# Performance work log

Hardware: AMD Instinct MI355X
Metric: run time of the kernel (lower is better)

Reference implementation:

```python
import jax, jax.numpy as jnp
import numpy as np

B, N, H, D = 8, 2048, 8, 64  # batch, seq, heads, head_dim
DM = H * D                   # model dim = 512


def setup_inputs() -> dict:
    key = jax.random.key(0)
    ks = jax.random.split(key, 9)
    std = 0.02
    return {
        "x": jax.random.normal(ks[0], (B, N, DM), dtype=jnp.float32),
        "Wq": jax.random.normal(ks[1], (H, D, D), dtype=jnp.float32) * std,
        "bq": jnp.zeros((H, D), dtype=jnp.float32),
        "Wk": jax.random.normal(ks[2], (H, D, D), dtype=jnp.float32) * std,
        "bk": jnp.zeros((H, D), dtype=jnp.float32),
        "Wv": jax.random.normal(ks[3], (H, D, D), dtype=jnp.float32) * std,
        "bv": jnp.zeros((H, D), dtype=jnp.float32),
        "Wp": jax.random.normal(ks[4], (DM, DM), dtype=jnp.float32) * std,
        "bp": jnp.zeros((DM,), dtype=jnp.float32),
    }


def reference(x, Wq, bq, Wk, bk, Wv, bv, Wp, bp):
    b, n, dm = x.shape
    # rearrange 'b n (h d) -> b h n d'
    xh = x.reshape(b, n, H, D).transpose(0, 2, 1, 3)  # [b,h,n,d]
    # per-head linear projections (torch Linear: y = x W^T + b), batched over heads
    q = jnp.einsum('bhnd,hed->bhne', xh, Wq) + bq[None, :, None, :]
    k = jnp.einsum('bhnd,hed->bhne', xh, Wk) + bk[None, :, None, :]
    v = jnp.einsum('bhnd,hed->bhne', xh, Wv) + bv[None, :, None, :]
    scale = 1.0 / jnp.sqrt(jnp.asarray(D, dtype=x.dtype))
    scores = jnp.einsum('bhqe,bhke->bhqk', q, k) * scale  # [b,h,n,n]
    attn = jax.nn.softmax(scores, axis=-1)
    out = jnp.einsum('bhqk,bhke->bhqe', attn, v)          # [b,h,n,d]
    # 'b h n d -> b n (h d)' then output projection
    out = out.transpose(0, 2, 1, 3).reshape(b, n, H * D)
    return out @ Wp.T + bp
```

## Files before the change

### kernel.cpp

```cpp
#include <hip/hip_runtime.h>
#include <hip/hip_bf16.h>

#define B_ 8
#define N_ 2048
#define H_ 8
#define DM_ 512
#define NT_ 32

typedef __bf16 bf16x8 __attribute__((ext_vector_type(8)));
typedef float f32x4 __attribute__((ext_vector_type(4)));
typedef float f32x16 __attribute__((ext_vector_type(16)));
typedef unsigned short us8 __attribute__((ext_vector_type(8)));
typedef unsigned short us4 __attribute__((ext_vector_type(4)));
typedef unsigned int u32x4 __attribute__((ext_vector_type(4)));

#define QSCALE 0.1803368801111204f

__device__ __forceinline__ int swz(int row, int byte_in_row) {
  return row * 128 + (byte_in_row ^ ((row & 7) << 4));
}

__device__ __forceinline__ unsigned short f2bf(float x) {
  __bf16 h = (__bf16)x;
  return __builtin_bit_cast(unsigned short, h);
}

__device__ __forceinline__ float fexp2(float x) {
#if __has_builtin(__builtin_amdgcn_exp2f)
  return __builtin_amdgcn_exp2f(x);
#else
  return exp2f(x);
#endif
}

__device__ __forceinline__ unsigned cvtpk(float a, float b) {
  unsigned r;
  asm("v_cvt_pk_bf16_f32 %0, %1, %2" : "=v"(r) : "v"(a), "v"(b));
  return r;
}

__device__ __forceinline__ void plswap(unsigned& a, unsigned& b) {
#if __has_builtin(__builtin_amdgcn_permlane32_swap)
  auto r = __builtin_amdgcn_permlane32_swap(a, b, false, false);
  a = r[0];
  b = r[1];
#else
  asm("v_permlane32_swap_b32 %0, %1" : "+v"(a), "+v"(b));
#endif
}

__device__ __forceinline__ f32x4 mfma16(bf16x8 a, bf16x8 b, f32x4 c) {
  return __builtin_amdgcn_mfma_f32_16x16x32_bf16(a, b, c, 0, 0, 0);
}
__device__ __forceinline__ f32x16 mfma32(bf16x8 a, bf16x8 b, f32x16 c) {
  return __builtin_amdgcn_mfma_f32_32x32x16_bf16(a, b, c, 0, 0, 0);
}

__device__ __forceinline__ bf16x8 ldg8(const unsigned short* p) {
  return *reinterpret_cast<const bf16x8*>(p);
}

__device__ __forceinline__ void stage_f32_tile(const float* __restrict__ src,
                                               int src_stride, char* dst, int t) {
#pragma unroll
  for (int rep = 0; rep < 4; ++rep) {
    int cid = rep * 256 + t;
    int row = cid >> 4, c4 = cid & 15;
    float4 v = *reinterpret_cast<const float4*>(src + (size_t)row * src_stride + c4 * 4);
    us4 o;
    o[0] = f2bf(v.x); o[1] = f2bf(v.y); o[2] = f2bf(v.z); o[3] = f2bf(v.w);
    *reinterpret_cast<us4*>(dst + row * 128 + ((c4 * 8) ^ ((row & 7) << 4))) = o;
  }
}

__device__ __forceinline__ void stage_bf16_tile(const unsigned short* __restrict__ src,
                                                int src_stride, char* dst, int t) {
#pragma unroll
  for (int rep = 0; rep < 2; ++rep) {
    int cid = rep * 256 + t;
    int row = cid >> 3, c = cid & 7;
    us8 v = *reinterpret_cast<const us8*>(src + (size_t)row * src_stride + c * 8);
    *reinterpret_cast<us8*>(dst + row * 128 + ((c * 16) ^ ((row & 7) << 4))) = v;
  }
}

__global__ __launch_bounds__(256, 4) void qkv_kernel(
    const float* __restrict__ x,
    const float* __restrict__ Wq, const float* __restrict__ bq,
    const float* __restrict__ Wk, const float* __restrict__ bk,
    const float* __restrict__ Wv, const float* __restrict__ bv,
    unsigned short* __restrict__ Qf, unsigned short* __restrict__ Kf,
    unsigned short* __restrict__ Vf) {
  __shared__ __align__(16) char sX[8192];
  __shared__ __align__(16) char sWq[8192];
  __shared__ __align__(16) char sWk[8192];
  __shared__ __align__(16) char sWv[8192];

  const int t = threadIdx.x;
  const int bh = blockIdx.y, h = bh & 7, b = bh >> 3;
  const int n0 = blockIdx.x * 64;
  const int lane = t & 63, w = t >> 6, g = lane >> 4, li = lane & 15;

  stage_f32_tile(x + ((size_t)(b * N_ + n0)) * DM_ + h * 64, DM_, sX, t);
  stage_f32_tile(Wq + (size_t)h * 4096, 64, sWq, t);
  stage_f32_tile(Wk + (size_t)h * 4096, 64, sWk, t);
  stage_f32_tile(Wv + (size_t)h * 4096, 64, sWv, t);
  __syncthreads();

  bf16x8 xa0 = *reinterpret_cast<const bf16x8*>(sX + swz(16 * w + li, 16 * g));
  bf16x8 xa1 = *reinterpret_cast<const bf16x8*>(sX + swz(16 * w + li, 64 + 16 * g));

  const size_t seg = (size_t)N_ * 64;
  const int qkbase =
      ((n0 >> 5) + (w >> 1)) * 2048 + (li >> 3) * 256 + (w & 1) * 128 + (li & 7);
  const int vbase =
      (n0 >> 6) * 4096 + w * 512 + (g >> 1) * 256 + 4 * (g & 1) + li * 8;

  unsigned short* Qs = Qf + (size_t)bh * seg;
  unsigned short* Ks = Kf + (size_t)bh * seg;
  unsigned short* Vs = Vf + (size_t)bh * seg;

#pragma unroll
  for (int c = 0; c < 4; ++c) {
    f32x4 a = {0.f, 0.f, 0.f, 0.f};
    bf16x8 b0 = *reinterpret_cast<const bf16x8*>(sWq + swz(c * 16 + li, 16 * g));
    bf16x8 b1 = *reinterpret_cast<const bf16x8*>(sWq + swz(c * 16 + li, 64 + 16 * g));
    a = mfma16(xa0, b0, a);
    a = mfma16(xa1, b1, a);
    float bb = bq[h * 64 + c * 16 + li];
#pragma unroll
    for (int i = 0; i < 4; ++i)
      Qs[qkbase + c * 512 + (4 * g + i) * 8] = f2bf((a[i] + bb) * QSCALE);
  }
#pragma unroll
  for (int c = 0; c < 4; ++c) {
    f32x4 a = {0.f, 0.f, 0.f, 0.f};
    bf16x8 b0 = *reinterpret_cast<const bf16x8*>(sWk + swz(c * 16 + li, 16 * g));
    bf16x8 b1 = *reinterpret_cast<const bf16x8*>(sWk + swz(c * 16 + li, 64 + 16 * g));
    a = mfma16(xa0, b0, a);
    a = mfma16(xa1, b1, a);
    float bb = bk[h * 64 + c * 16 + li];
#pragma unroll
    for (int i = 0; i < 4; ++i)
      Ks[qkbase + c * 512 + (4 * g + i) * 8] = f2bf(a[i] + bb);
  }
#pragma unroll
  for (int c = 0; c < 4; ++c) {
    f32x4 a = {0.f, 0.f, 0.f, 0.f};
    bf16x8 b0 = *reinterpret_cast<const bf16x8*>(sWv + swz(c * 16 + li, 16 * g));
    bf16x8 b1 = *reinterpret_cast<const bf16x8*>(sWv + swz(c * 16 + li, 64 + 16 * g));
    a = mfma16(xa0, b0, a);
    a = mfma16(xa1, b1, a);
    float bb = bv[h * 64 + c * 16 + li];
    us4 pk;
#pragma unroll
    for (int i = 0; i < 4; ++i) pk[i] = f2bf(a[i] + bb);
    *reinterpret_cast<us4*>(Vs + vbase + (c >> 1) * 2048 + (c & 1) * 128) = pk;
  }
}

__global__ __launch_bounds__(256, 3) void attn_kernel(
    const unsigned short* __restrict__ Qf, const unsigned short* __restrict__ Kf,
    const unsigned short* __restrict__ Vf, unsigned short* __restrict__ AOw) {
  const int t = threadIdx.x;
  const int lane = t & 63, w = t >> 6;
  const int lo = lane & 31;

  const int bid = blockIdx.x;
  const int work = (bid & 7) * 128 + (bid >> 3);
  const int bh = work >> 4;
  const int qb = (work & 15) * 4 + w;
  const int h = bh & 7, b = bh >> 3;

  const size_t seg = (size_t)N_ * 64;
  const unsigned short* qp = Qf + (size_t)bh * seg + qb * 2048 + lane * 8;
  const unsigned short* kp = Kf + (size_t)bh * seg + lane * 8;
  const unsigned short* vp = Vf + (size_t)bh * seg + lane * 8;

  bf16x8 qf[4];
#pragma unroll
  for (int dd = 0; dd < 4; ++dd) qf[dd] = ldg8(qp + dd * 512);

  bf16x8 kf[8], vf[8];
#pragma unroll
  for (int j = 0; j < 8; ++j) kf[j] = ldg8(kp + j * 512);

  f32x16 o0 = {}, o1 = {};
  float l = 0.f;

#pragma unroll 1
  for (int kt = 0; kt < NT_; ++kt) {
    {
      const unsigned short* vpt = vp + (size_t)kt * 4096;
#pragma unroll
      for (int j = 0; j < 8; ++j) vf[j] = ldg8(vpt + j * 512);
    }
    __builtin_amdgcn_sched_barrier(0);

    f32x16 s0 = {}, s1 = {};
    __builtin_amdgcn_s_setprio(1);
#pragma unroll
    for (int dd = 0; dd < 4; ++dd) {
      s0 = mfma32(kf[dd], qf[dd], s0);
      s1 = mfma32(kf[4 + dd], qf[dd], s1);
    }
    __builtin_amdgcn_s_setprio(0);

    if (kt + 1 < NT_) {
      const unsigned short* kpt = kp + (size_t)(kt + 1) * 4096;
#pragma unroll
      for (int j = 0; j < 8; ++j) kf[j] = ldg8(kpt + j * 512);
    }
    __builtin_amdgcn_sched_barrier(0);

    float ts0 = 0.f, ts1 = 0.f, ts2 = 0.f, ts3 = 0.f;
#pragma unroll
    for (int r = 0; r < 16; r += 4) {
      s0[r + 0] = fexp2(s0[r + 0]); ts0 += s0[r + 0];
      s0[r + 1] = fexp2(s0[r + 1]); ts1 += s0[r + 1];
      s0[r + 2] = fexp2(s0[r + 2]); ts2 += s0[r + 2];
      s0[r + 3] = fexp2(s0[r + 3]); ts3 += s0[r + 3];
      s1[r + 0] = fexp2(s1[r + 0]); ts0 += s1[r + 0];
      s1[r + 1] = fexp2(s1[r + 1]); ts1 += s1[r + 1];
      s1[r + 2] = fexp2(s1[r + 2]); ts2 += s1[r + 2];
      s1[r + 3] = fexp2(s1[r + 3]); ts3 += s1[r + 3];
    }
    l += (ts0 + ts1) + (ts2 + ts3);

    unsigned pl0[4], ph0[4], pl1[4], ph1[4];
#pragma unroll
    for (int qi = 0; qi < 4; ++qi) {
      pl0[qi] = cvtpk(s0[4 * qi + 0], s0[4 * qi + 1]);
      ph0[qi] = cvtpk(s0[4 * qi + 2], s0[4 * qi + 3]);
      pl1[qi] = cvtpk(s1[4 * qi + 0], s1[4 * qi + 1]);
      ph1[qi] = cvtpk(s1[4 * qi + 2], s1[4 * qi + 3]);
    }
    plswap(pl0[0], pl0[1]); plswap(ph0[0], ph0[1]);
    plswap(pl0[2], pl0[3]); plswap(ph0[2], ph0[3]);
    plswap(pl1[0], pl1[1]); plswap(ph1[0], ph1[1]);
    plswap(pl1[2], pl1[3]); plswap(ph1[2], ph1[3]);
    bf16x8 pf0, pf1, pf2, pf3;
    {
      u32x4 w0 = {pl0[0], ph0[0], pl0[1], ph0[1]};
      u32x4 w1 = {pl0[2], ph0[2], pl0[3], ph0[3]};
      u32x4 w2 = {pl1[0], ph1[0], pl1[1], ph1[1]};
      u32x4 w3 = {pl1[2], ph1[2], pl1[3], ph1[3]};
      pf0 = __builtin_bit_cast(bf16x8, w0);
      pf1 = __builtin_bit_cast(bf16x8, w1);
      pf2 = __builtin_bit_cast(bf16x8, w2);
      pf3 = __builtin_bit_cast(bf16x8, w3);
    }

    __builtin_amdgcn_s_setprio(1);
    o0 = mfma32(vf[0], pf0, o0);
    o1 = mfma32(vf[4], pf0, o1);
    o0 = mfma32(vf[1], pf1, o0);
    o1 = mfma32(vf[5], pf1, o1);
    o0 = mfma32(vf[2], pf2, o0);
    o1 = mfma32(vf[6], pf2, o1);
    o0 = mfma32(vf[3], pf3, o0);
    o1 = mfma32(vf[7], pf3, o1);
    __builtin_amdgcn_s_setprio(0);
  }

  l += __shfl_xor(l, 32);
  const int hi = lane >> 5;
  const float invl = 1.0f / l;
  unsigned short* aoptr =
      AOw + ((size_t)(b * N_) + qb * 32 + lo) * DM_ + h * 64 + 4 * hi;
#pragma unroll
  for (int qi = 0; qi < 4; ++qi) {
    us4 pk;
#pragma unroll
    for (int rr = 0; rr < 4; ++rr) pk[rr] = f2bf(o0[4 * qi + rr] * invl);
    *reinterpret_cast<us4*>(aoptr + 8 * qi) = pk;
  }
#pragma unroll
  for (int qi = 0; qi < 4; ++qi) {
    us4 pk;
#pragma unroll
    for (int rr = 0; rr < 4; ++rr) pk[rr] = f2bf(o1[4 * qi + rr] * invl);
    *reinterpret_cast<us4*>(aoptr + 32 + 8 * qi) = pk;
  }
}

__global__ __launch_bounds__(256, 4) void proj_kernel(
    const unsigned short* __restrict__ AOw, const float* __restrict__ Wp,
    const float* __restrict__ bp, float* __restrict__ out) {
  __shared__ __align__(16) char sA[8192];
  __shared__ __align__(16) char sB[8192];

  const int t = threadIdx.x;
  const int r0 = blockIdx.x * 64;
  const int i0 = blockIdx.y * 64;
  const int lane = t & 63, w = t >> 6, g = lane >> 4, li = lane & 15;

  f32x4 acc[4];
#pragma unroll
  for (int c = 0; c < 4; ++c) {
    acc[c][0] = 0.f; acc[c][1] = 0.f; acc[c][2] = 0.f; acc[c][3] = 0.f;
  }

  for (int jt = 0; jt < 8; ++jt) {
    __syncthreads();
    stage_bf16_tile(AOw + (size_t)r0 * DM_ + jt * 64, DM_, sA, t);
    stage_f32_tile(Wp + (size_t)i0 * DM_ + jt * 64, DM_, sB, t);
    __syncthreads();

    bf16x8 a0 = *reinterpret_cast<const bf16x8*>(sA + swz(16 * w + li, 16 * g));
    bf16x8 a1 = *reinterpret_cast<const bf16x8*>(sA + swz(16 * w + li, 64 + 16 * g));
#pragma unroll
    for (int c = 0; c < 4; ++c) {
      bf16x8 b0 = *reinterpret_cast<const bf16x8*>(sB + swz(c * 16 + li, 16 * g));
      bf16x8 b1 = *reinterpret_cast<const bf16x8*>(sB + swz(c * 16 + li, 64 + 16 * g));
      acc[c] = mfma16(a0, b0, acc[c]);
      acc[c] = mfma16(a1, b1, acc[c]);
    }
  }

#pragma unroll
  for (int c = 0; c < 4; ++c) {
    float bb = bp[i0 + c * 16 + li];
#pragma unroll
    for (int i = 0; i < 4; ++i)
      out[(size_t)(r0 + 16 * w + 4 * g + i) * DM_ + i0 + c * 16 + li] = acc[c][i] + bb;
  }
}

extern "C" void kernel_launch(void* const* d_in, const int* in_sizes, int n_in,
                              void* d_out, int out_size, void* d_ws, size_t ws_size,
                              hipStream_t stream) {
  const float* x  = (const float*)d_in[0];
  const float* Wq = (const float*)d_in[1];
  const float* bq = (const float*)d_in[2];
  const float* Wk = (const float*)d_in[3];
  const float* bk = (const float*)d_in[4];
  const float* Wv = (const float*)d_in[5];
  const float* bv = (const float*)d_in[6];
  const float* Wp = (const float*)d_in[7];
  const float* bp = (const float*)d_in[8];
  float* out = (float*)d_out;

  const size_t seg = (size_t)B_ * H_ * N_ * 64;
  unsigned short* Qf  = (unsigned short*)d_ws;
  unsigned short* Kf  = Qf + seg;
  unsigned short* Vf  = Kf + seg;
  unsigned short* AOw = Vf + seg;

  qkv_kernel<<<dim3(32, 64), 256, 0, stream>>>(x, Wq, bq, Wk, bk, Wv, bv, Qf, Kf, Vf);
  attn_kernel<<<dim3(1024), 256, 0, stream>>>(Qf, Kf, Vf, AOw);
  proj_kernel<<<dim3(256, 8), 256, 0, stream>>>(AOw, Wp, bp, out);
}
```

Baseline: 137.5 us.

## Split attention key range across warp pairs and merge partial outputs in LDS

Each attention block now handles two 32-row query tiles instead of four, with two warps per query tile each covering half of the key sequence. Partial output accumulators and row sums from the second key half are written to shared memory and added by the first half's warps before normalization. The grid doubles to 2048 blocks, giving more parallelism and shorter per-warp loops. In exchange, each query tile is loaded twice, and the kernel adds an LDS reduction, a block barrier and extra shared memory that may cut occupancy. The merge has no running-max rescaling, which is only correct because the softmax uses plain exp2 without a max.

```diff
diff --git a/kernel.cpp b/kernel.cpp
--- a/kernel.cpp
+++ b/kernel.cpp
@@ -6,6 +6,7 @@
 #define H_ 8
 #define DM_ 512
 #define NT_ 32
+#define NTH_ 16
 
 typedef __bf16 bf16x8 __attribute__((ext_vector_type(8)));
 typedef float f32x4 __attribute__((ext_vector_type(4)));
@@ -162,20 +163,25 @@
 __global__ __launch_bounds__(256, 3) void attn_kernel(
     const unsigned short* __restrict__ Qf, const unsigned short* __restrict__ Kf,
     const unsigned short* __restrict__ Vf, unsigned short* __restrict__ AOw) {
+  __shared__ float mo[32][2][64];
+  __shared__ float ml[2][64];
+
   const int t = threadIdx.x;
   const int lane = t & 63, w = t >> 6;
   const int lo = lane & 31;
+  const int qhalf = w & 1, khalf = w >> 1;
 
   const int bid = blockIdx.x;
-  const int work = (bid & 7) * 128 + (bid >> 3);
-  const int bh = work >> 4;
-  const int qb = (work & 15) * 4 + w;
+  const int work = (bid & 7) * 256 + (bid >> 3);
+  const int bh = work >> 5;
+  const int qc = work & 31;
+  const int qb = qc * 2 + qhalf;
   const int h = bh & 7, b = bh >> 3;
 
   const size_t seg = (size_t)N_ * 64;
   const unsigned short* qp = Qf + (size_t)bh * seg + qb * 2048 + lane * 8;
-  const unsigned short* kp = Kf + (size_t)bh * seg + lane * 8;
-  const unsigned short* vp = Vf + (size_t)bh * seg + lane * 8;
+  const unsigned short* kp = Kf + (size_t)bh * seg + (size_t)khalf * NTH_ * 4096 + lane * 8;
+  const unsigned short* vp = Vf + (size_t)bh * seg + (size_t)khalf * NTH_ * 4096 + lane * 8;
 
   bf16x8 qf[4];
 #pragma unroll
@@ -189,7 +195,7 @@
   float l = 0.f;
 
 #pragma unroll 1
-  for (int kt = 0; kt < NT_; ++kt) {
+  for (int kt = 0; kt < NTH_; ++kt) {
     {
       const unsigned short* vpt = vp + (size_t)kt * 4096;
 #pragma unroll
@@ -206,7 +212,7 @@
     }
     __builtin_amdgcn_s_setprio(0);
 
-    if (kt + 1 < NT_) {
+    if (kt + 1 < NTH_) {
       const unsigned short* kpt = kp + (size_t)(kt + 1) * 4096;
 #pragma unroll
       for (int j = 0; j < 8; ++j) kf[j] = ldg8(kpt + j * 512);
@@ -263,6 +269,24 @@
     __builtin_amdgcn_s_setprio(0);
   }
 
+  if (khalf) {
+#pragma unroll
+    for (int j = 0; j < 16; ++j) {
+      mo[j][qhalf][lane] = o0[j];
+      mo[16 + j][qhalf][lane] = o1[j];
+    }
+    ml[qhalf][lane] = l;
+  }
+  __syncthreads();
+  if (khalf) return;
+
+#pragma unroll
+  for (int j = 0; j < 16; ++j) {
+    o0[j] += mo[j][qhalf][lane];
+    o1[j] += mo[16 + j][qhalf][lane];
+  }
+  l += ml[qhalf][lane];
+
   l += __shfl_xor(l, 32);
   const int hi = lane >> 5;
   const float invl = 1.0f / l;
@@ -348,6 +372,6 @@
   unsigned short* AOw = Vf + seg;
 
   qkv_kernel<<<dim3(32, 64), 256, 0, stream>>>(x, Wq, bq, Wk, bk, Wv, bv, Qf, Kf, Vf);
-  attn_kernel<<<dim3(1024), 256, 0, stream>>>(Qf, Kf, Vf, AOw);
+  attn_kernel<<<dim3(2048), 256, 0, stream>>>(Qf, Kf, Vf, AOw);
   proj_kernel<<<dim3(256, 8), 256, 0, stream>>>(AOw, Wp, bp, out);
 }
```

After: 136.8 us. No clear change (-0.5%).

## Split attention KV range across four waves and reduce partials in shared memory

Applied to the files above, without the earlier changes.

Each block now handles a single 32-row query tile, and its four waves each process a quarter of the key/value sequence. The waves then combine their partial outputs and row sums through shared memory. This changes the parallelization from one wave per query tile to split-K within a block, launching 4x more blocks. The goal is shorter serial loops and better latency hiding. The cost is about 27KB of LDS per block, which may limit occupancy, plus a sync, a reduction, and Q loads repeated across waves. It relies on the existing no-max softmax, so partials add directly.

```diff
diff --git a/kernel.cpp b/kernel.cpp
--- a/kernel.cpp
+++ b/kernel.cpp
@@ -6,6 +6,7 @@
 #define H_ 8
 #define DM_ 512
 #define NT_ 32
+#define NTQ_ 8
 
 typedef __bf16 bf16x8 __attribute__((ext_vector_type(8)));
 typedef float f32x4 __attribute__((ext_vector_type(4)));
@@ -162,20 +163,25 @@
 __global__ __launch_bounds__(256, 3) void attn_kernel(
     const unsigned short* __restrict__ Qf, const unsigned short* __restrict__ Kf,
     const unsigned short* __restrict__ Vf, unsigned short* __restrict__ AOw) {
+  __shared__ float mo[32][3][64];
+  __shared__ float ml[3][64];
+
   const int t = threadIdx.x;
   const int lane = t & 63, w = t >> 6;
   const int lo = lane & 31;
 
   const int bid = blockIdx.x;
-  const int work = (bid & 7) * 128 + (bid >> 3);
-  const int bh = work >> 4;
-  const int qb = (work & 15) * 4 + w;
+  const int work = (bid & 7) * 512 + (bid >> 3);
+  const int bh = work >> 6;
+  const int qb = work & 63;
   const int h = bh & 7, b = bh >> 3;
 
   const size_t seg = (size_t)N_ * 64;
   const unsigned short* qp = Qf + (size_t)bh * seg + qb * 2048 + lane * 8;
-  const unsigned short* kp = Kf + (size_t)bh * seg + lane * 8;
-  const unsigned short* vp = Vf + (size_t)bh * seg + lane * 8;
+  const unsigned short* kp =
+      Kf + (size_t)bh * seg + (size_t)w * NTQ_ * 4096 + lane * 8;
+  const unsigned short* vp =
+      Vf + (size_t)bh * seg + (size_t)w * NTQ_ * 4096 + lane * 8;
 
   bf16x8 qf[4];
 #pragma unroll
@@ -189,7 +195,7 @@
   float l = 0.f;
 
 #pragma unroll 1
-  for (int kt = 0; kt < NT_; ++kt) {
+  for (int kt = 0; kt < NTQ_; ++kt) {
     {
       const unsigned short* vpt = vp + (size_t)kt * 4096;
 #pragma unroll
@@ -206,7 +212,7 @@
     }
     __builtin_amdgcn_s_setprio(0);
 
-    if (kt + 1 < NT_) {
+    if (kt + 1 < NTQ_) {
       const unsigned short* kpt = kp + (size_t)(kt + 1) * 4096;
 #pragma unroll
       for (int j = 0; j < 8; ++j) kf[j] = ldg8(kpt + j * 512);
@@ -263,6 +269,24 @@
     __builtin_amdgcn_s_setprio(0);
   }
 
+  if (w) {
+#pragma unroll
+    for (int j = 0; j < 16; ++j) {
+      mo[j][w - 1][lane] = o0[j];
+      mo[16 + j][w - 1][lane] = o1[j];
+    }
+    ml[w - 1][lane] = l;
+  }
+  __syncthreads();
+  if (w) return;
+
+#pragma unroll
+  for (int j = 0; j < 16; ++j) {
+    o0[j] += (mo[j][0][lane] + mo[j][1][lane]) + mo[j][2][lane];
+    o1[j] += (mo[16 + j][0][lane] + mo[16 + j][1][lane]) + mo[16 + j][2][lane];
+  }
+  l += (ml[0][lane] + ml[1][lane]) + ml[2][lane];
+
   l += __shfl_xor(l, 32);
   const int hi = lane >> 5;
   const float invl = 1.0f / l;
@@ -348,6 +372,6 @@
   unsigned short* AOw = Vf + seg;
 
   qkv_kernel<<<dim3(32, 64), 256, 0, stream>>>(x, Wq, bq, Wk, bk, Wv, bv, Qf, Kf, Vf);
-  attn_kernel<<<dim3(1024), 256, 0, stream>>>(Qf, Kf, Vf, AOw);
+  attn_kernel<<<dim3(4096), 256, 0, stream>>>(Qf, Kf, Vf, AOw);
   proj_kernel<<<dim3(256, 8), 256, 0, stream>>>(AOw, Wp, bp, out);
 }
```

Measured after the change: 138.9 us. About the same (+1.0%).
